# Performance work log

Measured on AMD Instinct MI355X. Metric: run time of the kernel, lower is better.

Reference implementation:

```python
import jax, jax.numpy as jnp
import numpy as np

B, S, D = 16, 2048, 64
SCALE = 1.0 / np.sqrt(np.float32(D))  # forward divides by sqrt(embedding_dim=64)


def setup_inputs() -> dict:
    key = jax.random.key(0)
    ks = jax.random.split(key, 7)
    return {
        "x": jax.random.normal(ks[0], (B, S, D), dtype=jnp.float32),
        "Wq": jax.random.normal(ks[1], (D, D), dtype=jnp.float32) * 0.02,
        "bq": jax.random.normal(ks[2], (D,), dtype=jnp.float32) * 0.02,
        "Wk": jax.random.normal(ks[3], (D, D), dtype=jnp.float32) * 0.02,
        "bk": jax.random.normal(ks[4], (D,), dtype=jnp.float32) * 0.02,
        "Wv": jax.random.normal(ks[5], (D, D), dtype=jnp.float32) * 0.02,
        "bv": jax.random.normal(ks[6], (D,), dtype=jnp.float32) * 0.02,
    }


def reference(x, Wq, bq, Wk, bk, Wv, bv):
    # Linear projections (weights stored [in, out], math-equivalent to nn.Linear)
    q = jnp.einsum("bsd,de->bse", x, Wq) + bq
    k = jnp.einsum("bsd,de->bse", x, Wk) + bk
    v = jnp.einsum("bsd,de->bse", x, Wv) + bv
    # Unfused scores: [B, S, S]
    scores = jnp.einsum("bqd,bkd->bqk", q, k) * jnp.float32(SCALE)
    causal = jnp.tril(jnp.ones((S, S), dtype=bool))  # mask[:S,:S]
    scores = jnp.where(causal, scores, jnp.float32(-jnp.inf))
    attn = jax.nn.softmax(scores, axis=-1)
    # dropout is identity in eval mode (reference baseline)
    out = jnp.einsum("bqk,bkd->bqd", attn, v)
    return out
```

## Files before the change

kernel.cpp:

```cpp
#include <hip/hip_runtime.h>

#define NB 16
#define SS 2048
#define DD 64

typedef __attribute__((ext_vector_type(8))) short short8;
typedef __attribute__((ext_vector_type(4))) float f32x4;

#define SCL2E 0.18033688011112042f

#define GLOAD_LDS(g, l) __builtin_amdgcn_global_load_lds( \
    (const __attribute__((address_space(1))) void*)(g),   \
    (__attribute__((address_space(3))) void*)(l), 16, 0, 0)

__device__ __forceinline__ short f2bf(float f) {
  union { float f; unsigned u; } v; v.f = f;
  unsigned r = (v.u + 0x7fffu + ((v.u >> 16) & 1u)) >> 16;
  return (short)r;
}

__device__ __forceinline__ unsigned cvtpk_bf16(float lo, float hi) {
  unsigned r;
  asm("v_cvt_pk_bf16_f32 %0, %1, %2" : "=v"(r) : "v"(lo), "v"(hi));
  return r;
}

__device__ __forceinline__ short8 load_a_frag_f32(const float* p) {
  float4 u = *(const float4*)p;
  float4 w = *(const float4*)(p + 4);
  short8 r;
  r[0] = f2bf(u.x); r[1] = f2bf(u.y); r[2] = f2bf(u.z); r[3] = f2bf(u.w);
  r[4] = f2bf(w.x); r[5] = f2bf(w.y); r[6] = f2bf(w.z); r[7] = f2bf(w.w);
  return r;
}

__global__ __launch_bounds__(768) void proj_kernel(
    const float* __restrict__ x,
    const float* __restrict__ Wq, const float* __restrict__ bq,
    const float* __restrict__ Wk, const float* __restrict__ bk,
    const float* __restrict__ Wv, const float* __restrict__ bv,
    ushort* __restrict__ qo, ushort* __restrict__ ko, ushort* __restrict__ vt)
{
  __shared__ __align__(16) ushort Wt[3][64][72];
  __shared__ __align__(16) ushort Vs[64][68];
  const int t = threadIdx.x;
#pragma unroll
  for (int i = 0; i < 4; ++i) {
    int idx = i * 3072 + t * 4;
    int m = idx >> 12, rem = idx & 4095;
    int kk = rem >> 6, n0 = rem & 63;
    const float* src = (m == 0 ? Wq : (m == 1 ? Wk : Wv));
    float4 w4 = *(const float4*)(src + rem);
    Wt[m][n0 + 0][kk] = (ushort)f2bf(w4.x);
    Wt[m][n0 + 1][kk] = (ushort)f2bf(w4.y);
    Wt[m][n0 + 2][kk] = (ushort)f2bf(w4.z);
    Wt[m][n0 + 3][kk] = (ushort)f2bf(w4.w);
  }
  __syncthreads();

  const int lane = t & 63, w = t >> 6;
  const int l15 = lane & 15, quad = lane >> 4;
  const int mm = w >> 2, rr = w & 3;
  const int g = blockIdx.x * 64 + rr * 16 + l15;

  short8 b0 = load_a_frag_f32(x + (size_t)g * 64 + quad * 8);
  short8 b1 = load_a_frag_f32(x + (size_t)g * 64 + 32 + quad * 8);

  const float* bp = (mm == 0 ? bq : (mm == 1 ? bk : bv));
  ushort* outp = (mm == 0 ? qo : ko);

#pragma unroll
  for (int nt = 0; nt < 4; ++nt) {
    const ushort* ap = &Wt[mm][nt * 16 + l15][quad * 8];
    short8 a0 = *(const short8*)ap;
    short8 a1 = *(const short8*)(ap + 32);
    f32x4 acc = {0.f, 0.f, 0.f, 0.f};
    acc = __builtin_amdgcn_mfma_f32_16x16x32_bf16(a0, b0, acc, 0, 0, 0);
    acc = __builtin_amdgcn_mfma_f32_16x16x32_bf16(a1, b1, acc, 0, 0, 0);
    float4 bb = *(const float4*)(bp + nt * 16 + quad * 4);
    uint2 pk;
    pk.x = cvtpk_bf16(acc[0] + bb.x, acc[1] + bb.y);
    pk.y = cvtpk_bf16(acc[2] + bb.z, acc[3] + bb.w);
    if (mm == 2) {
      *(uint2*)&Vs[rr * 16 + l15][nt * 16 + quad * 4] = pk;
    } else {
      int colb = (nt * 16 + quad * 4) * 2;
      if (mm == 1) colb ^= (g & 7) << 4;
      *(uint2*)((char*)outp + (size_t)g * 128 + colb) = pk;
    }
  }
  __syncthreads();
  if (t < 256) {
    const int batch = blockIdx.x >> 5;
    const int ktile = blockIdx.x & 31;
    const int d = t >> 2, j0 = (t & 3) * 16;
    ushort tmp[16];
#pragma unroll
    for (int j = 0; j < 16; ++j) tmp[j] = Vs[j0 + j][d];
    char* base = (char*)vt + ((size_t)batch * SS * DD + ktile * 4096) * 2 + d * 128;
    const int sw = (d & 7) << 4;
    *(int4*)(base + ((j0 * 2) ^ sw)) = ((int4*)tmp)[0];
    *(int4*)(base + ((j0 * 2 + 16) ^ sw)) = ((int4*)tmp)[1];
  }
}

__device__ __forceinline__ short8 build_pa(unsigned A0, unsigned A1,
                                           unsigned B0, unsigned B1, int quad) {
  int xA0 = __shfl_xor((int)A0, 32);
  int xA1 = __shfl_xor((int)A1, 32);
  int xB0 = __shfl_xor((int)B0, 32);
  int xB1 = __shfl_xor((int)B1, 32);
  const bool hi = quad >= 2;
  const bool odd = quad & 1;
  int Lo0 = hi ? xB0 : (int)A0;
  int Lo1 = hi ? xB1 : (int)A1;
  int Hi0 = hi ? (int)B0 : xA0;
  int Hi1 = hi ? (int)B1 : xA1;
  int xLo0 = __shfl_xor(Lo0, 16);
  int xLo1 = __shfl_xor(Lo1, 16);
  int xHi0 = __shfl_xor(Hi0, 16);
  int xHi1 = __shfl_xor(Hi1, 16);
  int4 wv;
  wv.x = odd ? xHi0 : Lo0;
  wv.y = odd ? xHi1 : Lo1;
  wv.z = odd ? Hi0 : xLo0;
  wv.w = odd ? Hi1 : xLo1;
  return *(short8*)&wv;
}

template<bool MASKED>
__device__ __forceinline__ void attn32(
    const f32x4 (&c)[2], float& l_acc, f32x4 (&acc)[4],
    const short8 (&vf)[4], int keybase, int qabs, int quad)
{
  unsigned pk[2][2];
#pragma unroll
  for (int c2 = 0; c2 < 2; ++c2) {
    float pe[4];
#pragma unroll
    for (int r = 0; r < 4; ++r) {
      float p = __builtin_amdgcn_exp2f(c[c2][r] * SCL2E);
      if (MASKED && (keybase + c2 * 16 + quad * 4 + r > qabs)) p = 0.f;
      pe[r] = p;
      l_acc += p;
    }
    pk[c2][0] = cvtpk_bf16(pe[0], pe[1]);
    pk[c2][1] = cvtpk_bf16(pe[2], pe[3]);
  }
  short8 pa = build_pa(pk[0][0], pk[0][1], pk[1][0], pk[1][1], quad);
  __builtin_amdgcn_s_setprio(1);
#pragma unroll
  for (int nt = 0; nt < 4; ++nt)
    acc[nt] = __builtin_amdgcn_mfma_f32_16x16x32_bf16(pa, vf[nt], acc[nt], 0, 0, 0);
  __builtin_amdgcn_s_setprio(0);
}

__device__ __forceinline__ void stage_tile(
    char* lds, const ushort* kg, const ushort* vt,
    size_t bbyte, int kt, int seg, int lane)
{
  const char* src = (seg < 4)
      ? (const char*)kg + bbyte + (size_t)kt * 8192 + seg * 2048
      : (const char*)vt + bbyte + (size_t)kt * 8192 + (seg - 4) * 2048;
  char* dst = lds + seg * 2048;
  GLOAD_LDS(src + lane * 16, dst);
  GLOAD_LDS(src + 1024 + lane * 16, dst + 1024);
}

__global__ __launch_bounds__(512) void attn_kernel(
    const ushort* __restrict__ qg, const ushort* __restrict__ kg,
    const ushort* __restrict__ vt, float* __restrict__ out)
{
  __shared__ __align__(16) char KV[2][16384];

  const int t = threadIdx.x, bid = blockIdx.x;
  const int batch = (bid & 7) * 2 + ((bid >> 3) & 1);
  const int qt = 31 - (bid >> 4);
  const int lane = t & 63, w = t >> 6;
  const int l15 = lane & 15, quad = lane >> 4;
  const int h = w >> 2;
  const int qgi = w & 3;
  const int qrow0 = qt * 64 + qgi * 16;
  const size_t bbase = (size_t)batch * SS * DD;
  const size_t bbyte = bbase * 2;

  const ushort* qp = qg + bbase + (size_t)(qrow0 + l15) * 64 + quad * 8;
  short8 a0 = *(const short8*)qp;
  short8 a1 = *(const short8*)(qp + 32);

  f32x4 acc[4];
  float l = 0.f;
#pragma unroll
  for (int nt = 0; nt < 4; ++nt) acc[nt] = (f32x4){0.f, 0.f, 0.f, 0.f};

  const int ktotal = qt + 1;
  const int qabs = qrow0 + l15;

  stage_tile(&KV[0][0], kg, vt, bbyte, 0, w, lane);
  __syncthreads();

  int cur = 0;
  for (int kt = 0; kt < ktotal; ++kt) {
    if (kt + 1 < ktotal)
      stage_tile(&KV[cur ^ 1][0], kg, vt, bbyte, kt + 1, w, lane);

    const char* Kb = &KV[cur][0];
    const char* Vb = &KV[cur][8192];
    short8 kf0[2], kf1[2], vf[4];
#pragma unroll
    for (int c2 = 0; c2 < 2; ++c2) {
      int row = (2 * h + c2) * 16 + l15;
      int sw = (row & 7) << 4;
      kf0[c2] = *(const short8*)(Kb + row * 128 + ((quad * 16) ^ sw));
      kf1[c2] = *(const short8*)(Kb + row * 128 + ((64 + quad * 16) ^ sw));
    }
#pragma unroll
    for (int nt = 0; nt < 4; ++nt) {
      int drow = nt * 16 + l15;
      int sv = (drow & 7) << 4;
      vf[nt] = *(const short8*)(Vb + drow * 128 + ((h * 64 + quad * 16) ^ sv));
    }

    f32x4 c[2];
    __builtin_amdgcn_s_setprio(1);
#pragma unroll
    for (int c2 = 0; c2 < 2; ++c2) {
      f32x4 z = {0.f, 0.f, 0.f, 0.f};
      c[c2] = __builtin_amdgcn_mfma_f32_16x16x32_bf16(kf0[c2], a0, z, 0, 0, 0);
      c[c2] = __builtin_amdgcn_mfma_f32_16x16x32_bf16(kf1[c2], a1, c[c2], 0, 0, 0);
    }
    __builtin_amdgcn_s_setprio(0);

    const int keybase = kt * 64 + h * 32;
    if (kt == ktotal - 1)
      attn32<true >(c, l, acc, vf, keybase, qabs, quad);
    else
      attn32<false>(c, l, acc, vf, keybase, qabs, quad);

    __syncthreads();
    cur ^= 1;
  }

  l += __shfl_xor(l, 16);
  l += __shfl_xor(l, 32);

  float* S = (float*)&KV[qgi >> 1][(qgi & 1) * 8192];
  if (h == 1) {
#pragma unroll
    for (int r = 0; r < 4; ++r)
#pragma unroll
      for (int nt = 0; nt < 4; ++nt)
        S[(quad * 4 + r) * 68 + nt * 16 + l15] = acc[nt][r];
    if (lane < 16) S[1088 + lane] = l;
  }
  __syncthreads();
  if (h == 0) {
    float lt = l + S[1088 + l15];
#pragma unroll
    for (int r = 0; r < 4; ++r) {
      float iv = 1.0f / __shfl(lt, quad * 4 + r);
      float* orow = out + bbase + (size_t)(qrow0 + quad * 4 + r) * 64 + l15;
#pragma unroll
      for (int nt = 0; nt < 4; ++nt)
        orow[nt * 16] = (acc[nt][r] + S[(quad * 4 + r) * 68 + nt * 16 + l15]) * iv;
    }
  }
}

extern "C" void kernel_launch(void* const* d_in, const int* in_sizes, int n_in,
                              void* d_out, int out_size, void* d_ws, size_t ws_size,
                              hipStream_t stream) {
  (void)in_sizes; (void)n_in; (void)out_size; (void)ws_size;
  const float* x  = (const float*)d_in[0];
  const float* Wq = (const float*)d_in[1];
  const float* bq = (const float*)d_in[2];
  const float* Wk = (const float*)d_in[3];
  const float* bk = (const float*)d_in[4];
  const float* Wv = (const float*)d_in[5];
  const float* bv = (const float*)d_in[6];
  float* out = (float*)d_out;

  ushort* qws = (ushort*)d_ws;
  ushort* kws = qws + (size_t)NB * SS * DD;
  ushort* vws = kws + (size_t)NB * SS * DD;

  proj_kernel<<<dim3(NB * SS / 64), dim3(768), 0, stream>>>(
      x, Wq, bq, Wk, bk, Wv, bv, qws, kws, vws);
  attn_kernel<<<dim3(NB * (SS / 64)), dim3(512), 0, stream>>>(
      qws, kws, vws, out);
}
```

Before: 106.3 us.

## Permute V^T storage so P fragments feed MFMA without cross-lane shuffles

Removes the build_pa routine, which used eight cross-lane shuffles per 32-key step to rearrange the softmax probabilities into the MFMA A-operand layout. The probabilities are now packed directly in register order. The V-transpose write is permuted with 8-byte chunk placement so the key ordering matches that register layout. A __syncthreads is also added before the epilogue reuses the shared buffer. In exchange the V^T stores become four 8-byte writes instead of two 16-byte writes, and the extra barrier adds a little cost.

```diff
diff --git a/kernel.cpp b/kernel.cpp
--- a/kernel.cpp
+++ b/kernel.cpp
@@ -99,33 +99,11 @@
     for (int j = 0; j < 16; ++j) tmp[j] = Vs[j0 + j][d];
     char* base = (char*)vt + ((size_t)batch * SS * DD + ktile * 4096) * 2 + d * 128;
     const int sw = (d & 7) << 4;
-    *(int4*)(base + ((j0 * 2) ^ sw)) = ((int4*)tmp)[0];
-    *(int4*)(base + ((j0 * 2 + 16) ^ sw)) = ((int4*)tmp)[1];
-  }
-}
-
-__device__ __forceinline__ short8 build_pa(unsigned A0, unsigned A1,
-                                           unsigned B0, unsigned B1, int quad) {
-  int xA0 = __shfl_xor((int)A0, 32);
-  int xA1 = __shfl_xor((int)A1, 32);
-  int xB0 = __shfl_xor((int)B0, 32);
-  int xB1 = __shfl_xor((int)B1, 32);
-  const bool hi = quad >= 2;
-  const bool odd = quad & 1;
-  int Lo0 = hi ? xB0 : (int)A0;
-  int Lo1 = hi ? xB1 : (int)A1;
-  int Hi0 = hi ? (int)B0 : xA0;
-  int Hi1 = hi ? (int)B1 : xA1;
-  int xLo0 = __shfl_xor(Lo0, 16);
-  int xLo1 = __shfl_xor(Lo1, 16);
-  int xHi0 = __shfl_xor(Hi0, 16);
-  int xHi1 = __shfl_xor(Hi1, 16);
-  int4 wv;
-  wv.x = odd ? xHi0 : Lo0;
-  wv.y = odd ? xHi1 : Lo1;
-  wv.z = odd ? Hi0 : xLo0;
-  wv.w = odd ? Hi1 : xLo1;
-  return *(short8*)&wv;
+    const int bcol = ((j0 >> 5) << 6) + (((j0 >> 4) & 1) << 3);
+#pragma unroll
+    for (int jj = 0; jj < 4; ++jj)
+      *(uint2*)(base + ((bcol + jj * 16) ^ sw)) = ((uint2*)tmp)[jj];
+  }
 }
 
 template<bool MASKED>
@@ -133,21 +111,23 @@
     const f32x4 (&c)[2], float& l_acc, f32x4 (&acc)[4],
     const short8 (&vf)[4], int keybase, int qabs, int quad)
 {
-  unsigned pk[2][2];
-#pragma unroll
-  for (int c2 = 0; c2 < 2; ++c2) {
+  unsigned pk[4];
+#pragma unroll
+  for (int ct = 0; ct < 2; ++ct) {
     float pe[4];
 #pragma unroll
     for (int r = 0; r < 4; ++r) {
-      float p = __builtin_amdgcn_exp2f(c[c2][r] * SCL2E);
-      if (MASKED && (keybase + c2 * 16 + quad * 4 + r > qabs)) p = 0.f;
+      float p = __builtin_amdgcn_exp2f(c[ct][r] * SCL2E);
+      if (MASKED && (keybase + ct * 16 + quad * 4 + r > qabs)) p = 0.f;
       pe[r] = p;
       l_acc += p;
     }
-    pk[c2][0] = cvtpk_bf16(pe[0], pe[1]);
-    pk[c2][1] = cvtpk_bf16(pe[2], pe[3]);
-  }
-  short8 pa = build_pa(pk[0][0], pk[0][1], pk[1][0], pk[1][1], quad);
+    pk[ct * 2 + 0] = cvtpk_bf16(pe[0], pe[1]);
+    pk[ct * 2 + 1] = cvtpk_bf16(pe[2], pe[3]);
+  }
+  int4 w4;
+  w4.x = (int)pk[0]; w4.y = (int)pk[1]; w4.z = (int)pk[2]; w4.w = (int)pk[3];
+  short8 pa = *(short8*)&w4;
   __builtin_amdgcn_s_setprio(1);
 #pragma unroll
   for (int nt = 0; nt < 4; ++nt)
@@ -243,6 +223,8 @@
 
   l += __shfl_xor(l, 16);
   l += __shfl_xor(l, 32);
+
+  __syncthreads();
 
   float* S = (float*)&KV[qgi >> 1][(qgi & 1) * 8192];
   if (h == 1) {
```

Result: faster. 99.40 us (median of 2 runs) (-6.5%).
